# Performance work log

Hardware: AMD Instinct MI355X
Metric: run time of the kernel (lower is better)

The kernel has to match this reference:

```python
import jax, jax.numpy as jnp
import numpy as np

B, L, H, V = 32, 4096, 512, 32000


def setup_inputs() -> dict:
    key = jax.random.key(0)
    ks = jax.random.split(key, 16)
    s = 0.02  # weight init scale
    return {
        "input_token": jax.random.normal(ks[0], (B, H), jnp.float32),
        "h0": jax.random.normal(ks[1], (B, H), jnp.float32),
        "c0": jax.random.normal(ks[2], (B, H), jnp.float32),
        "document_output": jax.random.normal(ks[3], (B, L, H), jnp.float32),
        "document_mask": jax.random.randint(ks[4], (B, L), 0, 2, jnp.int32),
        "W_ih": jax.random.normal(ks[5], (4 * H, H), jnp.float32) * s,
        "W_hh": jax.random.normal(ks[6], (4 * H, H), jnp.float32) * s,
        "b_ih": jax.random.normal(ks[7], (4 * H,), jnp.float32) * s,
        "b_hh": jax.random.normal(ks[8], (4 * H,), jnp.float32) * s,
        "W1_w": jax.random.normal(ks[9], (H, H), jnp.float32) * s,
        "W1_b": jax.random.normal(ks[10], (H,), jnp.float32) * s,
        "W2_w": jax.random.normal(ks[11], (H, H), jnp.float32) * s,
        "W2_b": jax.random.normal(ks[12], (H,), jnp.float32) * s,
        "u1": jax.random.normal(ks[13], (H,), jnp.float32),
        "Wout_w": jax.random.normal(ks[14], (V, 2 * H), jnp.float32) * s,
        "Wout_b": jax.random.normal(ks[15], (V,), jnp.float32) * s,
    }


def reference(input_token, h0, c0, document_output, document_mask,
              W_ih, W_hh, b_ih, b_hh, W1_w, W1_b, W2_w, W2_b, u1,
              Wout_w, Wout_b):
    # Single LSTM step (torch gate order: i, f, g, o)
    gates = input_token @ W_ih.T + b_ih + h0 @ W_hh.T + b_hh  # (B, 4H)
    i, f, g, o = jnp.split(gates, 4, axis=-1)
    c = jax.nn.sigmoid(f) * c0 + jax.nn.sigmoid(i) * jnp.tanh(g)
    h = jax.nn.sigmoid(o) * jnp.tanh(c)  # (B, H)

    # Additive (Bahdanau) attention over document positions
    q = h @ W1_w.T + W1_b                                     # (B, H)
    k = document_output @ W2_w.T + W2_b                       # (B, L, H)
    combined = jnp.tanh(q[:, None, :] + k)                    # (B, L, H)
    scores = jnp.einsum("blh,h->bl", combined, u1)            # (B, L)
    scores = jnp.where(document_mask.astype(bool), scores, -jnp.inf)
    attn = jax.nn.softmax(scores, axis=1)                     # (B, L)
    context = jnp.einsum("bl,blh->bh", attn, document_output)  # (B, H)

    combined_context = jnp.concatenate([h, context], axis=1)  # (B, 2H)
    output = combined_context @ Wout_w.T + Wout_b             # (B, V)
    return output, h, c
```

## Files before the change

### kernel.cpp

```cpp
#include <hip/hip_runtime.h>
#include <hip/hip_bf16.h>
#include <math.h>

#define B_  32
#define L_  4096
#define H_  512
#define V_  32000
#define MBLK 128

typedef __attribute__((ext_vector_type(4))) float f32x4;
typedef __attribute__((ext_vector_type(2))) float f32x2;
typedef __attribute__((ext_vector_type(8))) short short8;
typedef __attribute__((ext_vector_type(4))) unsigned short u16x4;

__device__ __forceinline__ unsigned short bf16_rne(float x){
  union { float f; unsigned int u; } v; v.f = x;
  unsigned int u = v.u;
  return (unsigned short)((u + 0x7FFFu + ((u >> 16) & 1u)) >> 16);
}
__device__ __forceinline__ float bf16_f32(unsigned short h){
  union { unsigned int u; float f; } v; v.u = ((unsigned int)h) << 16;
  return v.f;
}
__device__ __forceinline__ float tanh_cheap(float x){
  float e = __expf(x + x);
  return 1.0f - 2.0f * __builtin_amdgcn_rcpf(e + 1.0f);
}
__device__ __forceinline__ short8 cvt8(f32x4 a, f32x4 b){
  union { __hip_bfloat162 h[4]; short8 s; } u;
  u.h[0] = __float22bfloat162_rn(make_float2(a[0], a[1]));
  u.h[1] = __float22bfloat162_rn(make_float2(a[2], a[3]));
  u.h[2] = __float22bfloat162_rn(make_float2(b[0], b[1]));
  u.h[3] = __float22bfloat162_rn(make_float2(b[2], b[3]));
  return u.s;
}

__global__ __launch_bounds__(256) void k_convert_w2(
    const float* __restrict__ w2, unsigned short* __restrict__ hi){
  int i = (blockIdx.x * 256 + threadIdx.x) * 4;
  f32x4 v = *(const f32x4*)(w2 + i);
  u16x4 h;
  #pragma unroll
  for (int e = 0; e < 4; ++e) h[e] = bf16_rne(v[e]);
  *(u16x4*)(hi + i) = h;
}

__global__ __launch_bounds__(256) void k_gates(
    const float* __restrict__ x, const float* __restrict__ h0,
    const float* __restrict__ Wih, const float* __restrict__ Whh,
    const float* __restrict__ bih, const float* __restrict__ bhh,
    float* __restrict__ gates){
  __shared__ float sx[H_], sh[H_];
  int b = blockIdx.y, t = threadIdx.x;
  sx[t] = x[b*H_ + t]; sx[t+256] = x[b*H_ + t + 256];
  sh[t] = h0[b*H_ + t]; sh[t+256] = h0[b*H_ + t + 256];
  __syncthreads();
  int j = blockIdx.x * 256 + t;
  const float* wi = Wih + j*H_;
  const float* wh = Whh + j*H_;
  float acc = bih[j] + bhh[j];
  #pragma unroll 4
  for (int k = 0; k < H_; k += 4) {
    f32x4 a = *(const f32x4*)(wi + k);
    f32x4 c = *(const f32x4*)(wh + k);
    acc += a[0]*sx[k] + a[1]*sx[k+1] + a[2]*sx[k+2] + a[3]*sx[k+3];
    acc += c[0]*sh[k] + c[1]*sh[k+1] + c[2]*sh[k+2] + c[3]*sh[k+3];
  }
  gates[b*2048 + j] = acc;
}

__global__ __launch_bounds__(256) void k_lstm(
    const float* __restrict__ gates, const float* __restrict__ c0,
    float* __restrict__ out_h, float* __restrict__ out_c, float* __restrict__ cc,
    unsigned short* __restrict__ ccb){
  int idx = blockIdx.x * 256 + threadIdx.x;
  int b = idx >> 9, hh = idx & 511;
  const float* g = gates + b*2048;
  float gi = g[hh], gf = g[512+hh], gg = g[1024+hh], go = g[1536+hh];
  float si = 1.f/(1.f+expf(-gi));
  float sf = 1.f/(1.f+expf(-gf));
  float so = 1.f/(1.f+expf(-go));
  float c = sf * c0[idx] + si * tanhf(gg);
  float h = so * tanhf(c);
  out_h[idx] = h; out_c[idx] = c;
  cc[b*1024 + hh] = h;
  ccb[b*1024 + hh] = bf16_rne(h);
}

__global__ __launch_bounds__(256) void k_q(
    const float* __restrict__ cc, const float* __restrict__ W1,
    const float* __restrict__ b1, float* __restrict__ q){
  __shared__ float shh[H_];
  int b = blockIdx.y, t = threadIdx.x;
  shh[t] = cc[b*1024 + t]; shh[t+256] = cc[b*1024 + t + 256];
  __syncthreads();
  int j = blockIdx.x*256 + t;
  const float* w = W1 + j*H_;
  float acc = b1[j];
  #pragma unroll 4
  for (int k = 0; k < H_; k += 4){
    f32x4 a = *(const f32x4*)(w + k);
    acc += a[0]*shh[k] + a[1]*shh[k+1] + a[2]*shh[k+2] + a[3]*shh[k+3];
  }
  q[b*H_ + j] = acc;
}

__global__ __launch_bounds__(512, 2) void k_scores_ctx(
    const float* __restrict__ doc, const unsigned short* __restrict__ w2hi,
    const float* __restrict__ qv,
    const float* __restrict__ w2b, const float* __restrict__ u1,
    const int* __restrict__ mask,
    float* __restrict__ ctxp, float* __restrict__ bm, float* __restrict__ bs){
  __shared__ short Adoc[8][MBLK][8][8];
  __shared__ float2 s_qu[512];
  __shared__ float s_part[8][MBLK];
  __shared__ float e_arr[MBLK];
  __shared__ float wred[4];
  __shared__ float cpart[2][512];
  int t = threadIdx.x;
  int row0 = blockIdx.x * MBLK;
  int b = row0 >> 12;
  s_qu[t] = make_float2(qv[b*512 + t] + w2b[t], u1[t]);

  int sr = t >> 2;
  int sg = t & 3;
  const float* dbase = doc + (((long)(row0 + sr)) << 9) + sg*16;
  int wc0 = (2*sg)     ^ (sr & 7);
  int wc1 = (2*sg + 1) ^ (sr & 7);

  int wave = t >> 6, lane = t & 63;
  int lrow = lane & 15, lk = lane >> 4;
  int sw = lrow & 7;
  int j0 = wave * 64;
  const unsigned short* pbh = w2hi + (j0 + lrow)*512 + lk*8;

  f32x4 acc[8][4];
  #pragma unroll
  for (int mt = 0; mt < 8; ++mt)
    #pragma unroll
    for (int jj = 0; jj < 4; ++jj)
      acc[mt][jj] = (f32x4){0.f, 0.f, 0.f, 0.f};

  {
    f32x4 v0 = *(const f32x4*)(dbase);
    f32x4 v1 = *(const f32x4*)(dbase + 4);
    f32x4 v2 = *(const f32x4*)(dbase + 8);
    f32x4 v3 = *(const f32x4*)(dbase + 12);
    *(short8*)&Adoc[0][sr][wc0][0] = cvt8(v0, v1);
    *(short8*)&Adoc[0][sr][wc1][0] = cvt8(v2, v3);
  }
  __syncthreads();

  for (int s = 0; s < 8; ++s){
    short8 bh[8];
    {
      int ko = s*64;
      #pragma unroll
      for (int jj = 0; jj < 4; ++jj){
        bh[jj]   = *(const short8*)(pbh + jj*8192 + ko);
        bh[4+jj] = *(const short8*)(pbh + jj*8192 + ko + 32);
      }
    }
    f32x4 pf0, pf1, pf2, pf3;
    if (s < 7){
      const float* p = dbase + (s+1)*64;
      pf0 = *(const f32x4*)(p);
      pf1 = *(const f32x4*)(p + 4);
      pf2 = *(const f32x4*)(p + 8);
      pf3 = *(const f32x4*)(p + 12);
    }
    #pragma unroll
    for (int ktl = 0; ktl < 2; ++ktl){
      short8 a[8];
      #pragma unroll
      for (int mt = 0; mt < 8; ++mt)
        a[mt] = *(const short8*)&Adoc[s][mt*16 + lrow][(ktl*4 + lk) ^ sw][0];
      #pragma unroll
      for (int jj = 0; jj < 4; ++jj)
        #pragma unroll
        for (int mt = 0; mt < 8; ++mt)
          acc[mt][jj] = __builtin_amdgcn_mfma_f32_16x16x32_bf16(bh[ktl*4 + jj], a[mt], acc[mt][jj], 0, 0, 0);
    }
    if (s < 7){
      *(short8*)&Adoc[s+1][sr][wc0][0] = cvt8(pf0, pf1);
      *(short8*)&Adoc[s+1][sr][wc1][0] = cvt8(pf2, pf3);
    }
    __syncthreads();
  }

  #pragma unroll
  for (int mt = 0; mt < 8; ++mt){
    float p = 0.f;
    #pragma unroll
    for (int jj = 0; jj < 4; ++jj){
      #pragma unroll
      for (int r = 0; r < 4; ++r){
        int j = j0 + jj*16 + lk*4 + r;
        float2 qu = s_qu[j];
        p += tanh_cheap(acc[mt][jj][r] + qu.x) * qu.y;
      }
    }
    p += __shfl_xor(p, 16);
    p += __shfl_xor(p, 32);
    if (lane < 16) s_part[wave][mt*16 + lrow] = p;
  }
  __syncthreads();

  float sl = 0.f;
  bool ok = false;
  if (t < MBLK){
    #pragma unroll
    for (int w = 0; w < 8; ++w) sl += s_part[w][t];
    ok = mask[row0 + t] != 0;
    sl = ok ? sl : -INFINITY;
    float m = sl;
    #pragma unroll
    for (int o = 1; o < 64; o <<= 1) m = fmaxf(m, __shfl_xor(m, o));
    if (lane == 0) wred[wave] = m;
  }
  __syncthreads();
  if (t < MBLK){
    float mb = fmaxf(wred[0], wred[1]);
    float e = ok ? __expf(sl - mb) : 0.f;
    float es = e;
    #pragma unroll
    for (int o = 1; o < 64; o <<= 1) es += __shfl_xor(es, o);
    if (lane == 0) wred[2 + wave] = es;
    e_arr[t] = e;
    if (t == 0) bm[blockIdx.x] = mb;
  }
  __syncthreads();
  if (t == 0) bs[blockIdx.x] = wred[2] + wred[3];

  {
    int p = t & 255, half = t >> 8;
    int h0 = 2*p;
    int sstep = h0 >> 6;
    int c = (h0 >> 3) & 7;
    int e = h0 & 7;
    float a0 = 0.f, a1 = 0.f;
    int l0 = half * 64;
    #pragma unroll 8
    for (int l = l0; l < l0 + 64; ++l){
      int cp = c ^ (l & 7);
      unsigned v = *(const unsigned*)((const char*)&Adoc[sstep][l][cp][0] + e*2);
      float el = e_arr[l];
      a0 += el * bf16_f32((unsigned short)(v & 0xffff));
      a1 += el * bf16_f32((unsigned short)(v >> 16));
    }
    cpart[half][2*p]   = a0;
    cpart[half][2*p+1] = a1;
  }
  __syncthreads();
  ctxp[(long)blockIdx.x * 512 + t] = cpart[0][t] + cpart[1][t];
}

__global__ __launch_bounds__(512) void k_combine(
    const float* __restrict__ ctxp, const float* __restrict__ bm,
    const float* __restrict__ bs, unsigned short* __restrict__ ccb){
  __shared__ float sw[32];
  __shared__ float sT;
  int b = blockIdx.x, t = threadIdx.x;
  if (t < 32){
    float m = bm[b*32 + t], s = bs[b*32 + t];
    float M = m;
    #pragma unroll
    for (int o = 1; o < 32; o <<= 1) M = fmaxf(M, __shfl_xor(M, o));
    float w = (m == -INFINITY) ? 0.f : __expf(m - M);
    float ts = s * w;
    #pragma unroll
    for (int o = 1; o < 32; o <<= 1) ts += __shfl_xor(ts, o);
    sw[t] = w;
    if (t == 0) sT = ts;
  }
  __syncthreads();
  float invT = 1.f / sT;
  const float* cp = ctxp + (long)b*32*512 + t;
  float acc = 0.f;
  #pragma unroll 8
  for (int blk = 0; blk < 32; ++blk) acc += cp[blk*512] * sw[blk];
  ccb[b*1024 + 512 + t] = bf16_rne(acc * invT);
}

__global__ __launch_bounds__(256) void k_out(
    const unsigned short* __restrict__ ccb, const float* __restrict__ Wout,
    const float* __restrict__ bout, float* __restrict__ out){
  __shared__ short Ccb[32][128][8];
  __shared__ float s_out[32][65];
  int t = threadIdx.x, wave = t >> 6, lane = t & 63;
  int v0 = blockIdx.x * 64;
  #pragma unroll
  for (int i = 0; i < 16; ++i){
    int c16 = i*256 + t;
    int bb = c16 >> 7, ch = c16 & 127;
    int chsw = (ch & ~7) | ((ch & 7) ^ (bb & 7));
    *(short8*)&Ccb[bb][chsw][0] = *(const short8*)(ccb + c16*8);
  }
  __syncthreads();

  int lrow = lane & 15, lk = lane >> 4;
  int vrow = v0 + wave*16 + lrow;
  const float* wptr = Wout + (long)vrow*1024 + lk*8;
  f32x4 acc[2];
  acc[0] = (f32x4){0.f,0.f,0.f,0.f};
  acc[1] = (f32x4){0.f,0.f,0.f,0.f};
  int sw = lrow & 7;
  f32x4 w0 = *(const f32x4*)(wptr);
  f32x4 w1 = *(const f32x4*)(wptr + 4);
  #pragma unroll 4
  for (int ks = 0; ks < 32; ++ks){
    f32x4 nw0, nw1;
    if (ks < 31){
      nw0 = *(const f32x4*)(wptr + (ks+1)*32);
      nw1 = *(const f32x4*)(wptr + (ks+1)*32 + 4);
    }
    short8 bfrag = cvt8(w0, w1);
    int ch = ks*4 + lk;
    int chsw = (ch & ~7) | ((ch & 7) ^ sw);
    short8 a0 = *(const short8*)&Ccb[lrow][chsw][0];
    short8 a1 = *(const short8*)&Ccb[16 + lrow][chsw][0];
    acc[0] = __builtin_amdgcn_mfma_f32_16x16x32_bf16(bfrag, a0, acc[0], 0, 0, 0);
    acc[1] = __builtin_amdgcn_mfma_f32_16x16x32_bf16(bfrag, a1, acc[1], 0, 0, 0);
    w0 = nw0; w1 = nw1;
  }
  #pragma unroll
  for (int mt = 0; mt < 2; ++mt)
    #pragma unroll
    for (int r = 0; r < 4; ++r)
      s_out[mt*16 + lrow][wave*16 + lk*4 + r] = acc[mt][r];
  __syncthreads();
  int vcol = t & 63, bq = t >> 6;
  float bo = bout[v0 + vcol];
  #pragma unroll
  for (int bb = 0; bb < 8; ++bb){
    int brow = bb*4 + bq;
    out[(long)brow*V_ + v0 + vcol] = s_out[brow][vcol] + bo;
  }
}

extern "C" void kernel_launch(void* const* d_in, const int* in_sizes, int n_in,
                              void* d_out, int out_size, void* d_ws, size_t ws_size,
                              hipStream_t stream){
  const float* x    = (const float*)d_in[0];
  const float* h0   = (const float*)d_in[1];
  const float* c0   = (const float*)d_in[2];
  const float* doc  = (const float*)d_in[3];
  const int*   mask = (const int*)d_in[4];
  const float* Wih  = (const float*)d_in[5];
  const float* Whh  = (const float*)d_in[6];
  const float* bih  = (const float*)d_in[7];
  const float* bhh  = (const float*)d_in[8];
  const float* W1   = (const float*)d_in[9];
  const float* b1   = (const float*)d_in[10];
  const float* W2   = (const float*)d_in[11];
  const float* b2   = (const float*)d_in[12];
  const float* u1   = (const float*)d_in[13];
  const float* Wo   = (const float*)d_in[14];
  const float* bo   = (const float*)d_in[15];
  float* out  = (float*)d_out;
  float* outh = out + B_*V_;
  float* outc = outh + B_*H_;

  float* ws    = (float*)d_ws;
  float* gates = ws;
  float* q     = gates + 65536;
  float* cc    = q + 16384;
  float* ctxp  = cc + 32768;
  float* bm    = ctxp + 524288;
  float* bs    = bm + 1024;
  unsigned short* w2hi = (unsigned short*)(bs + 1024);
  unsigned short* ccb  = w2hi + 262144;

  hipLaunchKernelGGL(k_convert_w2, dim3(256), dim3(256), 0, stream, W2, w2hi);
  hipLaunchKernelGGL(k_gates, dim3(8, 32), dim3(256), 0, stream, x, h0, Wih, Whh, bih, bhh, gates);
  hipLaunchKernelGGL(k_lstm, dim3(64), dim3(256), 0, stream, gates, c0, outh, outc, cc, ccb);
  hipLaunchKernelGGL(k_q, dim3(2, 32), dim3(256), 0, stream, cc, W1, b1, q);
  hipLaunchKernelGGL(k_scores_ctx, dim3(1024), dim3(512), 0, stream, doc, w2hi, q, b2, u1, mask, ctxp, bm, bs);
  hipLaunchKernelGGL(k_combine, dim3(32), dim3(512), 0, stream, ctxp, bm, bs, ccb);
  hipLaunchKernelGGL(k_out, dim3(500), dim3(256), 0, stream, ccb, Wo, bo, out);
}
```

Baseline: 237.0 us.

## Double thread count in scores kernel and widen output GEMM blocks with direct stores

k_scores_ctx now launches 1024 threads per block. Each wave covers a 64x64 tile instead of 64x128, which halves the accumulator registers per thread, and the per-stage document loads and context reduction are spread across more threads. k_out now uses 512-thread blocks covering 128 vocab rows each. It drops the shared-memory transpose and writes results with vector stores straight from the MFMA accumulators. The goal is more latency hiding through more waves in flight, at the cost of a bigger block and more W2 fragment reloads per wave. The output stores now follow the accumulator layout, which may coalesce less well.

```diff
diff --git a/kernel.cpp b/kernel.cpp
--- a/kernel.cpp
+++ b/kernel.cpp
@@ -105,7 +105,7 @@
   q[b*H_ + j] = acc;
 }
 
-__global__ __launch_bounds__(512, 2) void k_scores_ctx(
+__global__ __launch_bounds__(1024, 1) void k_scores_ctx(
     const float* __restrict__ doc, const unsigned short* __restrict__ w2hi,
     const float* __restrict__ qv,
     const float* __restrict__ w2b, const float* __restrict__ u1,
@@ -116,27 +116,28 @@
   __shared__ float s_part[8][MBLK];
   __shared__ float e_arr[MBLK];
   __shared__ float wred[4];
-  __shared__ float cpart[2][512];
+  __shared__ float cpart[4][512];
   int t = threadIdx.x;
   int row0 = blockIdx.x * MBLK;
   int b = row0 >> 12;
-  s_qu[t] = make_float2(qv[b*512 + t] + w2b[t], u1[t]);
-
-  int sr = t >> 2;
-  int sg = t & 3;
-  const float* dbase = doc + (((long)(row0 + sr)) << 9) + sg*16;
-  int wc0 = (2*sg)     ^ (sr & 7);
-  int wc1 = (2*sg + 1) ^ (sr & 7);
+  if (t < 512) s_qu[t] = make_float2(qv[b*512 + t] + w2b[t], u1[t]);
+
+  int sr = t >> 3;
+  int sg = t & 7;
+  const float* dbase = doc + (((long)(row0 + sr)) << 9) + sg*8;
+  int wc = sg ^ (sr & 7);
 
   int wave = t >> 6, lane = t & 63;
   int lrow = lane & 15, lk = lane >> 4;
   int sw = lrow & 7;
-  int j0 = wave * 64;
+  int jh = wave & 7, mh = wave >> 3;
+  int j0 = jh * 64;
+  int m0 = mh * 64;
   const unsigned short* pbh = w2hi + (j0 + lrow)*512 + lk*8;
 
-  f32x4 acc[8][4];
-  #pragma unroll
-  for (int mt = 0; mt < 8; ++mt)
+  f32x4 acc[4][4];
+  #pragma unroll
+  for (int mt = 0; mt < 4; ++mt)
     #pragma unroll
     for (int jj = 0; jj < 4; ++jj)
       acc[mt][jj] = (f32x4){0.f, 0.f, 0.f, 0.f};
@@ -144,52 +145,41 @@
   {
     f32x4 v0 = *(const f32x4*)(dbase);
     f32x4 v1 = *(const f32x4*)(dbase + 4);
-    f32x4 v2 = *(const f32x4*)(dbase + 8);
-    f32x4 v3 = *(const f32x4*)(dbase + 12);
-    *(short8*)&Adoc[0][sr][wc0][0] = cvt8(v0, v1);
-    *(short8*)&Adoc[0][sr][wc1][0] = cvt8(v2, v3);
+    *(short8*)&Adoc[0][sr][wc][0] = cvt8(v0, v1);
   }
   __syncthreads();
 
   for (int s = 0; s < 8; ++s){
-    short8 bh[8];
-    {
-      int ko = s*64;
-      #pragma unroll
-      for (int jj = 0; jj < 4; ++jj){
-        bh[jj]   = *(const short8*)(pbh + jj*8192 + ko);
-        bh[4+jj] = *(const short8*)(pbh + jj*8192 + ko + 32);
-      }
-    }
-    f32x4 pf0, pf1, pf2, pf3;
+    f32x4 pf0, pf1;
     if (s < 7){
       const float* p = dbase + (s+1)*64;
       pf0 = *(const f32x4*)(p);
       pf1 = *(const f32x4*)(p + 4);
-      pf2 = *(const f32x4*)(p + 8);
-      pf3 = *(const f32x4*)(p + 12);
     }
     #pragma unroll
     for (int ktl = 0; ktl < 2; ++ktl){
-      short8 a[8];
+      short8 bh[4];
+      int ko = s*64 + ktl*32;
       #pragma unroll
-      for (int mt = 0; mt < 8; ++mt)
-        a[mt] = *(const short8*)&Adoc[s][mt*16 + lrow][(ktl*4 + lk) ^ sw][0];
+      for (int jj = 0; jj < 4; ++jj)
+        bh[jj] = *(const short8*)(pbh + jj*8192 + ko);
+      short8 a[4];
+      #pragma unroll
+      for (int mt = 0; mt < 4; ++mt)
+        a[mt] = *(const short8*)&Adoc[s][m0 + mt*16 + lrow][(ktl*4 + lk) ^ sw][0];
       #pragma unroll
       for (int jj = 0; jj < 4; ++jj)
         #pragma unroll
-        for (int mt = 0; mt < 8; ++mt)
-          acc[mt][jj] = __builtin_amdgcn_mfma_f32_16x16x32_bf16(bh[ktl*4 + jj], a[mt], acc[mt][jj], 0, 0, 0);
-    }
-    if (s < 7){
-      *(short8*)&Adoc[s+1][sr][wc0][0] = cvt8(pf0, pf1);
-      *(short8*)&Adoc[s+1][sr][wc1][0] = cvt8(pf2, pf3);
-    }
+        for (int mt = 0; mt < 4; ++mt)
+          acc[mt][jj] = __builtin_amdgcn_mfma_f32_16x16x32_bf16(bh[jj], a[mt], acc[mt][jj], 0, 0, 0);
+    }
+    if (s < 7)
+      *(short8*)&Adoc[s+1][sr][wc][0] = cvt8(pf0, pf1);
     __syncthreads();
   }
 
   #pragma unroll
-  for (int mt = 0; mt < 8; ++mt){
+  for (int mt = 0; mt < 4; ++mt){
     float p = 0.f;
     #pragma unroll
     for (int jj = 0; jj < 4; ++jj){
@@ -202,7 +192,7 @@
     }
     p += __shfl_xor(p, 16);
     p += __shfl_xor(p, 32);
-    if (lane < 16) s_part[wave][mt*16 + lrow] = p;
+    if (lane < 16) s_part[jh][m0 + mt*16 + lrow] = p;
   }
   __syncthreads();
 
@@ -233,26 +223,27 @@
   if (t == 0) bs[blockIdx.x] = wred[2] + wred[3];
 
   {
-    int p = t & 255, half = t >> 8;
+    int p = t & 255, quarter = t >> 8;
     int h0 = 2*p;
     int sstep = h0 >> 6;
     int c = (h0 >> 3) & 7;
     int e = h0 & 7;
     float a0 = 0.f, a1 = 0.f;
-    int l0 = half * 64;
+    int l0 = quarter * 32;
     #pragma unroll 8
-    for (int l = l0; l < l0 + 64; ++l){
+    for (int l = l0; l < l0 + 32; ++l){
       int cp = c ^ (l & 7);
       unsigned v = *(const unsigned*)((const char*)&Adoc[sstep][l][cp][0] + e*2);
       float el = e_arr[l];
       a0 += el * bf16_f32((unsigned short)(v & 0xffff));
       a1 += el * bf16_f32((unsigned short)(v >> 16));
     }
-    cpart[half][2*p]   = a0;
-    cpart[half][2*p+1] = a1;
-  }
-  __syncthreads();
-  ctxp[(long)blockIdx.x * 512 + t] = cpart[0][t] + cpart[1][t];
+    cpart[quarter][2*p]   = a0;
+    cpart[quarter][2*p+1] = a1;
+  }
+  __syncthreads();
+  if (t < 512)
+    ctxp[(long)blockIdx.x * 512 + t] = cpart[0][t] + cpart[1][t] + cpart[2][t] + cpart[3][t];
 }
 
 __global__ __launch_bounds__(512) void k_combine(
@@ -282,16 +273,15 @@
   ccb[b*1024 + 512 + t] = bf16_rne(acc * invT);
 }
 
-__global__ __launch_bounds__(256) void k_out(
+__global__ __launch_bounds__(512, 2) void k_out(
     const unsigned short* __restrict__ ccb, const float* __restrict__ Wout,
     const float* __restrict__ bout, float* __restrict__ out){
   __shared__ short Ccb[32][128][8];
-  __shared__ float s_out[32][65];
   int t = threadIdx.x, wave = t >> 6, lane = t & 63;
-  int v0 = blockIdx.x * 64;
-  #pragma unroll
-  for (int i = 0; i < 16; ++i){
-    int c16 = i*256 + t;
+  int v0 = blockIdx.x * 128;
+  #pragma unroll
+  for (int i = 0; i < 8; ++i){
+    int c16 = i*512 + t;
     int bb = c16 >> 7, ch = c16 & 127;
     int chsw = (ch & ~7) | ((ch & 7) ^ (bb & 7));
     *(short8*)&Ccb[bb][chsw][0] = *(const short8*)(ccb + c16*8);
@@ -323,18 +313,16 @@
     acc[1] = __builtin_amdgcn_mfma_f32_16x16x32_bf16(bfrag, a1, acc[1], 0, 0, 0);
     w0 = nw0; w1 = nw1;
   }
-  #pragma unroll
-  for (int mt = 0; mt < 2; ++mt)
-    #pragma unroll
-    for (int r = 0; r < 4; ++r)
-      s_out[mt*16 + lrow][wave*16 + lk*4 + r] = acc[mt][r];
-  __syncthreads();
-  int vcol = t & 63, bq = t >> 6;
-  float bo = bout[v0 + vcol];
-  #pragma unroll
-  for (int bb = 0; bb < 8; ++bb){
-    int brow = bb*4 + bq;
-    out[(long)brow*V_ + v0 + vcol] = s_out[brow][vcol] + bo;
+  int vcol = v0 + wave*16 + lk*4;
+  f32x4 bo4 = *(const f32x4*)&bout[vcol];
+  #pragma unroll
+  for (int mt = 0; mt < 2; ++mt){
+    f32x4 res;
+    res[0] = acc[mt][0] + bo4[0];
+    res[1] = acc[mt][1] + bo4[1];
+    res[2] = acc[mt][2] + bo4[2];
+    res[3] = acc[mt][3] + bo4[3];
+    *(f32x4*)&out[(long)(mt*16 + lrow)*V_ + vcol] = res;
   }
 }
 
@@ -375,7 +363,7 @@
   hipLaunchKernelGGL(k_gates, dim3(8, 32), dim3(256), 0, stream, x, h0, Wih, Whh, bih, bhh, gates);
   hipLaunchKernelGGL(k_lstm, dim3(64), dim3(256), 0, stream, gates, c0, outh, outc, cc, ccb);
   hipLaunchKernelGGL(k_q, dim3(2, 32), dim3(256), 0, stream, cc, W1, b1, q);
-  hipLaunchKernelGGL(k_scores_ctx, dim3(1024), dim3(512), 0, stream, doc, w2hi, q, b2, u1, mask, ctxp, bm, bs);
+  hipLaunchKernelGGL(k_scores_ctx, dim3(1024), dim3(1024), 0, stream, doc, w2hi, q, b2, u1, mask, ctxp, bm, bs);
   hipLaunchKernelGGL(k_combine, dim3(32), dim3(512), 0, stream, ctxp, bm, bs, ccb);
-  hipLaunchKernelGGL(k_out, dim3(500), dim3(256), 0, stream, ccb, Wo, bo, out);
-}
+  hipLaunchKernelGGL(k_out, dim3(250), dim3(512), 0, stream, ccb, Wo, bo, out);
+}
```

Result: slower. 304.8 us (+28.6%).

## Pre-transpose W2 into k-chunk-major bf16 layout and widen k_out blocks

Applied to the files above, without the earlier changes.

W2 is converted to bf16 in a layout where each 8-element k-chunk is stored contiguously across output rows. This makes the per-lane B-fragment loads in k_scores_ctx hit adjacent addresses instead of stride-512 rows. k_out now uses 512-thread blocks covering 128 vocab columns, drops the LDS staging buffer and barrier, and writes outputs directly as float4 with the bias added in registers. The direct stores are less coalesced across lanes than the old staged row writes, and the larger block changes occupancy.

```diff
diff --git a/kernel.cpp b/kernel.cpp
--- a/kernel.cpp
+++ b/kernel.cpp
@@ -36,13 +36,13 @@
 }
 
 __global__ __launch_bounds__(256) void k_convert_w2(
-    const float* __restrict__ w2, unsigned short* __restrict__ hi){
-  int i = (blockIdx.x * 256 + threadIdx.x) * 4;
-  f32x4 v = *(const f32x4*)(w2 + i);
-  u16x4 h;
-  #pragma unroll
-  for (int e = 0; e < 4; ++e) h[e] = bf16_rne(v[e]);
-  *(u16x4*)(hi + i) = h;
+    const float* __restrict__ w2, unsigned short* __restrict__ w2t){
+  int idx = blockIdx.x * 256 + threadIdx.x;
+  int j = idx & 511, kc = idx >> 9;
+  const float* src = w2 + j*512 + kc*8;
+  f32x4 a = *(const f32x4*)src;
+  f32x4 b = *(const f32x4*)(src + 4);
+  *(short8*)(w2t + (long)(kc*512 + j)*8) = cvt8(a, b);
 }
 
 __global__ __launch_bounds__(256) void k_gates(
@@ -106,7 +106,7 @@
 }
 
 __global__ __launch_bounds__(512, 2) void k_scores_ctx(
-    const float* __restrict__ doc, const unsigned short* __restrict__ w2hi,
+    const float* __restrict__ doc, const unsigned short* __restrict__ w2t,
     const float* __restrict__ qv,
     const float* __restrict__ w2b, const float* __restrict__ u1,
     const int* __restrict__ mask,
@@ -132,7 +132,7 @@
   int lrow = lane & 15, lk = lane >> 4;
   int sw = lrow & 7;
   int j0 = wave * 64;
-  const unsigned short* pbh = w2hi + (j0 + lrow)*512 + lk*8;
+  const unsigned short* pbh = w2t + (long)(lk*512 + j0 + lrow)*8;
 
   f32x4 acc[8][4];
   #pragma unroll
@@ -154,11 +154,11 @@
   for (int s = 0; s < 8; ++s){
     short8 bh[8];
     {
-      int ko = s*64;
+      const unsigned short* pb = pbh + (long)s*8*512*8;
       #pragma unroll
       for (int jj = 0; jj < 4; ++jj){
-        bh[jj]   = *(const short8*)(pbh + jj*8192 + ko);
-        bh[4+jj] = *(const short8*)(pbh + jj*8192 + ko + 32);
+        bh[jj]   = *(const short8*)(pb + jj*128);
+        bh[4+jj] = *(const short8*)(pb + 4*512*8 + jj*128);
       }
     }
     f32x4 pf0, pf1, pf2, pf3;
@@ -282,16 +282,15 @@
   ccb[b*1024 + 512 + t] = bf16_rne(acc * invT);
 }
 
-__global__ __launch_bounds__(256) void k_out(
+__global__ __launch_bounds__(512, 2) void k_out(
     const unsigned short* __restrict__ ccb, const float* __restrict__ Wout,
     const float* __restrict__ bout, float* __restrict__ out){
   __shared__ short Ccb[32][128][8];
-  __shared__ float s_out[32][65];
   int t = threadIdx.x, wave = t >> 6, lane = t & 63;
-  int v0 = blockIdx.x * 64;
+  int v0 = blockIdx.x * 128;
   #pragma unroll
-  for (int i = 0; i < 16; ++i){
-    int c16 = i*256 + t;
+  for (int i = 0; i < 8; ++i){
+    int c16 = i*512 + t;
     int bb = c16 >> 7, ch = c16 & 127;
     int chsw = (ch & ~7) | ((ch & 7) ^ (bb & 7));
     *(short8*)&Ccb[bb][chsw][0] = *(const short8*)(ccb + c16*8);
@@ -323,18 +322,16 @@
     acc[1] = __builtin_amdgcn_mfma_f32_16x16x32_bf16(bfrag, a1, acc[1], 0, 0, 0);
     w0 = nw0; w1 = nw1;
   }
+  int vcol = v0 + wave*16 + lk*4;
+  f32x4 bo4 = *(const f32x4*)&bout[vcol];
   #pragma unroll
-  for (int mt = 0; mt < 2; ++mt)
-    #pragma unroll
-    for (int r = 0; r < 4; ++r)
-      s_out[mt*16 + lrow][wave*16 + lk*4 + r] = acc[mt][r];
-  __syncthreads();
-  int vcol = t & 63, bq = t >> 6;
-  float bo = bout[v0 + vcol];
-  #pragma unroll
-  for (int bb = 0; bb < 8; ++bb){
-    int brow = bb*4 + bq;
-    out[(long)brow*V_ + v0 + vcol] = s_out[brow][vcol] + bo;
+  for (int mt = 0; mt < 2; ++mt){
+    f32x4 res;
+    res[0] = acc[mt][0] + bo4[0];
+    res[1] = acc[mt][1] + bo4[1];
+    res[2] = acc[mt][2] + bo4[2];
+    res[3] = acc[mt][3] + bo4[3];
+    *(f32x4*)&out[(long)(mt*16 + lrow)*V_ + vcol] = res;
   }
 }
 
@@ -368,14 +365,14 @@
   float* ctxp  = cc + 32768;
   float* bm    = ctxp + 524288;
   float* bs    = bm + 1024;
-  unsigned short* w2hi = (unsigned short*)(bs + 1024);
-  unsigned short* ccb  = w2hi + 262144;
-
-  hipLaunchKernelGGL(k_convert_w2, dim3(256), dim3(256), 0, stream, W2, w2hi);
+  unsigned short* w2t = (unsigned short*)(bs + 1024);
+  unsigned short* ccb = w2t + 262144;
+
+  hipLaunchKernelGGL(k_convert_w2, dim3(128), dim3(256), 0, stream, W2, w2t);
   hipLaunchKernelGGL(k_gates, dim3(8, 32), dim3(256), 0, stream, x, h0, Wih, Whh, bih, bhh, gates);
   hipLaunchKernelGGL(k_lstm, dim3(64), dim3(256), 0, stream, gates, c0, outh, outc, cc, ccb);
   hipLaunchKernelGGL(k_q, dim3(2, 32), dim3(256), 0, stream, cc, W1, b1, q);
-  hipLaunchKernelGGL(k_scores_ctx, dim3(1024), dim3(512), 0, stream, doc, w2hi, q, b2, u1, mask, ctxp, bm, bs);
+  hipLaunchKernelGGL(k_scores_ctx, dim3(1024), dim3(512), 0, stream, doc, w2t, q, b2, u1, mask, ctxp, bm, bs);
   hipLaunchKernelGGL(k_combine, dim3(32), dim3(512), 0, stream, ctxp, bm, bs, ccb);
-  hipLaunchKernelGGL(k_out, dim3(500), dim3(256), 0, stream, ccb, Wo, bo, out);
-}
+  hipLaunchKernelGGL(k_out, dim3(250), dim3(512), 0, stream, ccb, Wo, bo, out);
+}
```

Result: faster. 225.9 us (-4.7%).
